# Kernel tuning notes

Measured on AMD Instinct MI355X. Metric: run time of the kernel, lower is better.

Reference implementation:

```python
import jax, jax.numpy as jnp
import numpy as np


def setup_inputs() -> dict:
    key = jax.random.key(0)
    ks = jax.random.split(key, 5)
    S, B, H, L = 512, 64, 1024, 2
    scale = 0.1
    return {
        "x": jax.random.normal(ks[0], (S, B, H), dtype=jnp.float32),
        "h0": jnp.zeros((L, B, H), dtype=jnp.float32),
        "c0": jnp.zeros((L, B, H), dtype=jnp.float32),
        "Wx": jax.random.uniform(ks[1], (L, 4 * H, H), minval=-scale, maxval=scale, dtype=jnp.float32),
        "Wh": jax.random.uniform(ks[2], (L, 4 * H, H), minval=-scale, maxval=scale, dtype=jnp.float32),
        "bx": jax.random.uniform(ks[3], (L, 4 * H), minval=-scale, maxval=scale, dtype=jnp.float32),
        "bh": jax.random.uniform(ks[4], (L, 4 * H), minval=-scale, maxval=scale, dtype=jnp.float32),
    }


def _cell(x_t, h_prev, c_prev, Wx_l, Wh_l, bx_l, bh_l, H):
    # gates: [B, 4H]; chunk order per source: f, i, o, c_ex
    gates = x_t @ Wx_l.T + bx_l + h_prev @ Wh_l.T + bh_l
    f, i, o, c_ex = jnp.split(gates, 4, axis=1)
    f = jax.nn.sigmoid(f)
    i = jax.nn.sigmoid(i)
    o = jax.nn.sigmoid(o)
    c_ex = jnp.tanh(c_ex)
    c = f * c_prev + i * c_ex
    h = o * jnp.tanh(c)
    return h, c


def reference(x, h0, c0, Wx, Wh, bx, bh):
    # x: [S, B, H]; h0/c0: [L, B, H]; Wx/Wh: [L, 4H, H]; bx/bh: [L, 4H]
    L = h0.shape[0]
    H = h0.shape[-1]

    def step(carry, x_t):
        h_all, c_all = carry  # each [L, B, H]
        out = x_t
        hs, cs = [], []
        for l in range(L):  # small fixed layer count
            h, c = _cell(out, h_all[l], c_all[l], Wx[l], Wh[l], bx[l], bh[l], H)
            out = h  # dropout is identity in eval mode
            hs.append(h)
            cs.append(c)
        return (jnp.stack(hs, 0), jnp.stack(cs, 0)), out

    (h_fin, c_fin), ys = jax.lax.scan(step, (h0, c0), x)
    return ys, (h_fin, c_fin)
```

## Files before the change

kernel.cpp:

```cpp
#include <hip/hip_runtime.h>

typedef __bf16 bf16_t;
typedef __bf16 bf16x8 __attribute__((ext_vector_type(8)));
typedef __bf16 bf16x4 __attribute__((ext_vector_type(4)));
typedef float  f32x4  __attribute__((ext_vector_type(4)));
typedef unsigned long long u64;

#define S_LEN 512
#define BATCH 64
#define HID 1024
#define BH (BATCH*HID)
#define G4 (4*HID)
#define NBLK 256
#define LBLK 128
#define NTHR 512
#define CSTRIDE 32
#define NCHK 8

__device__ __forceinline__ float sigmoid_f(float x) { return 1.f / (1.f + __expf(-x)); }
__device__ __forceinline__ float tanh_f(float x) {
    float e = __expf(-2.f * fabsf(x));
    float t = (1.f - e) / (1.f + e);
    return x >= 0.f ? t : -t;
}

__device__ __forceinline__ bf16x8 cvt8(const float* p) {
    float4 a = *reinterpret_cast<const float4*>(p);
    float4 b = *reinterpret_cast<const float4*>(p + 4);
    bf16x8 r;
    r[0] = (bf16_t)a.x; r[1] = (bf16_t)a.y; r[2] = (bf16_t)a.z; r[3] = (bf16_t)a.w;
    r[4] = (bf16_t)b.x; r[5] = (bf16_t)b.y; r[6] = (bf16_t)b.z; r[7] = (bf16_t)b.w;
    return r;
}

__device__ __forceinline__ void wait_chunk(const unsigned* cp, unsigned thr) {
    if (__hip_atomic_load(cp, __ATOMIC_RELAXED, __HIP_MEMORY_SCOPE_AGENT) < thr) {
        do { __builtin_amdgcn_s_sleep(2); }
        while (__hip_atomic_load(cp, __ATOMIC_RELAXED, __HIP_MEMORY_SCOPE_AGENT) < thr);
    }
    asm volatile("" ::: "memory");
}

__device__ __forceinline__ void gemm_phase_chunked(
    const bf16_t* __restrict__ abase, const unsigned* __restrict__ cbase, unsigned thr,
    int grbase, const unsigned char* __restrict__ lds_w,
    int kh, int quad, int r16, int ff, f32x4& acc0, f32x4& acc1)
{
    bf16x8 af[8];
    wait_chunk(&cbase[(4 * kh) * CSTRIDE], thr);
    if (!ff) __builtin_amdgcn_fence(__ATOMIC_ACQUIRE, "agent");
    #pragma unroll
    for (int j = 0; j < 4; ++j)
        af[j] = *reinterpret_cast<const bf16x8*>(abase + j * 32);
    #pragma unroll
    for (int c = 0; c < 4; ++c) {
        if (c < 3) {
            wait_chunk(&cbase[(4 * kh + c + 1) * CSTRIDE], thr);
            if (!ff) __builtin_amdgcn_fence(__ATOMIC_ACQUIRE, "agent");
            #pragma unroll
            for (int j = 0; j < 4; ++j)
                af[((c + 1) & 1) * 4 + j] =
                    *reinterpret_cast<const bf16x8*>(abase + (4 * (c + 1) + j) * 32);
        }
        #pragma unroll
        for (int j = 0; j < 4; ++j) {
            int ks = 4 * c + j;
            int gr = grbase + kh * 64 + ks * 4 + quad;
            bf16x8 b0 = *reinterpret_cast<const bf16x8*>(&lds_w[gr * 512 + r16 * 16]);
            bf16x8 b1 = *reinterpret_cast<const bf16x8*>(&lds_w[gr * 512 + (16 + r16) * 16]);
            acc0 = __builtin_amdgcn_mfma_f32_16x16x32_bf16(af[(c & 1) * 4 + j], b0, acc0, 0, 0, 0);
            acc1 = __builtin_amdgcn_mfma_f32_16x16x32_bf16(af[(c & 1) * 4 + j], b1, acc1, 0, 0, 0);
        }
    }
}

__global__ void prep_kernel(const float* __restrict__ h0,
                            bf16_t* __restrict__ h0buf, bf16_t* __restrict__ h1buf,
                            unsigned* __restrict__ cnt, int mask0, int mask1) {
    int gtid = blockIdx.x * blockDim.x + threadIdx.x;
    int gsz  = gridDim.x * blockDim.x;
    if (gtid < 2 * NCHK) cnt[gtid * CSTRIDE] = 0u;
    for (int i = gtid; i < BH; i += gsz) {
        h0buf[(size_t)mask0 * BH + i] = (bf16_t)h0[i];
        h1buf[(size_t)mask1 * BH + i] = (bf16_t)h0[BH + i];
    }
}

__global__ __launch_bounds__(NTHR, 2) void lstm_persistent(
    const float* __restrict__ x,
    const float* __restrict__ c0,
    const float* __restrict__ Wx,
    const float* __restrict__ Wh,
    const float* __restrict__ bx,
    const float* __restrict__ bh,
    float* __restrict__ out,
    bf16_t* __restrict__ h0buf,
    bf16_t* __restrict__ h1buf,
    unsigned* __restrict__ cnt,
    int ff, int mask0, int mask1)
{
    __shared__ __attribute__((aligned(16))) unsigned char lds_w[256 * 512];
    __shared__ __attribute__((aligned(16))) float lds_red[8 * 256];
    __shared__ __attribute__((aligned(16))) float lds_hf[BATCH * 8];

    const int tid  = threadIdx.x;
    const int bid  = blockIdx.x;
    const int l    = bid >> 7;
    const int ug8  = bid & 127;
    const int lane = tid & 63;
    const int wv   = tid >> 6;
    const int mt   = wv >> 1;
    const int kh   = wv & 1;
    const int quad = lane >> 4;
    const int r16  = lane & 15;

    float* ys   = out;
    float* hfin = out + (size_t)S_LEN * BH;
    float* cfin = hfin + 2 * BH;

    {
        const float* WxL = Wx + (size_t)l * G4 * HID;
        const float* WhL = Wh + (size_t)l * G4 * HID;
        for (int ch = tid; ch < 32 * 256; ch += NTHR) {
            int row = ch & 31;
            int gr  = ch >> 5;
            int ul = row >> 2, g = row & 3;
            size_t R = (size_t)g * HID + 8 * ug8 + ul;
            const float* src = (gr < 128) ? (WxL + R * HID + (size_t)gr * 8)
                                          : (WhL + R * HID + (size_t)(gr - 128) * 8);
            *reinterpret_cast<bf16x8*>(&lds_w[gr * 512 + row * 16]) = cvt8(src);
        }
    }

    const int b_loc  = lane >> 2;
    const int uu     = lane & 3;
    const int b_glob = 16 * mt + b_loc;
    const int u_loc  = 4 * kh + uu;
    const int u_glob = 8 * ug8 + u_loc;

    float bias_r[4];
    #pragma unroll
    for (int gi = 0; gi < 4; ++gi) {
        int R = gi * HID + u_glob;
        bias_r[gi] = bx[l * G4 + R] + bh[l * G4 + R];
    }
    float c_reg = c0[(size_t)l * BH + (size_t)b_glob * HID + u_glob];

    bf16_t* pubbuf = (l == 0) ? h0buf : h1buf;
    const int pubmask = (l == 0) ? mask0 : mask1;
    const unsigned* cnt0 = cnt;
    const unsigned* cnt1 = cnt + NCHK * CSTRIDE;
    unsigned* mycnt = &cnt[(l * NCHK + (ug8 >> 4)) * CSTRIDE];
    __syncthreads();

    const int arow_off = (16 * mt + r16) * HID + kh * 512 + quad * 8;

    bf16x8 axp[16];
    if (l == 0) {
        const float* arow = x + arow_off;
        #pragma unroll
        for (int ks = 0; ks < 16; ++ks) axp[ks] = cvt8(arow + ks * 32);
    }

    for (int t = 0; t < S_LEN; ++t) {
        f32x4 acc0 = {0.f, 0.f, 0.f, 0.f};
        f32x4 acc1 = {0.f, 0.f, 0.f, 0.f};

        if (l == 0) {
            #pragma unroll
            for (int ks = 0; ks < 16; ++ks) {
                int gr = kh * 64 + ks * 4 + quad;
                bf16x8 b0 = *reinterpret_cast<const bf16x8*>(&lds_w[gr * 512 + r16 * 16]);
                bf16x8 b1 = *reinterpret_cast<const bf16x8*>(&lds_w[gr * 512 + (16 + r16) * 16]);
                acc0 = __builtin_amdgcn_mfma_f32_16x16x32_bf16(axp[ks], b0, acc0, 0, 0, 0);
                acc1 = __builtin_amdgcn_mfma_f32_16x16x32_bf16(axp[ks], b1, acc1, 0, 0, 0);
            }
            const bf16_t* ah = h0buf + (size_t)((t - 1) & mask0) * BH + arow_off;
            gemm_phase_chunked(ah, cnt0, (unsigned)(16 * t), 128, lds_w,
                               kh, quad, r16, ff, acc0, acc1);
        } else {
            const bf16_t* ax = h0buf + (size_t)(t & mask0) * BH + arow_off;
            gemm_phase_chunked(ax, cnt0, (unsigned)(16 * (t + 1)), 0, lds_w,
                               kh, quad, r16, ff, acc0, acc1);
            const bf16_t* ah = h1buf + (size_t)((t - 1) & mask1) * BH + arow_off;
            gemm_phase_chunked(ah, cnt1, (unsigned)(16 * t), 128, lds_w,
                               kh, quad, r16, ff, acc0, acc1);
        }

        {
            f32x4 ship = kh ? acc0 : acc1;
            *reinterpret_cast<f32x4*>(&lds_red[wv * 256 + lane * 4]) = ship;
            __syncthreads();
            f32x4 part = *reinterpret_cast<const f32x4*>(&lds_red[(wv ^ 1) * 256 + lane * 4]);
            f32x4 keep = kh ? acc1 : acc0;
            acc0 = keep + part;
        }

        {
            const int quad_s = b_loc >> 2;
            const int reg_s  = b_loc & 3;
            float gsum[4];
            #pragma unroll
            for (int gi = 0; gi < 4; ++gi) {
                int lane_s = (quad_s << 4) | (4 * uu + gi);
                float v0 = __shfl(acc0[0], lane_s, 64);
                float v1 = __shfl(acc0[1], lane_s, 64);
                float v2 = __shfl(acc0[2], lane_s, 64);
                float v3 = __shfl(acc0[3], lane_s, 64);
                float v  = (reg_s == 0) ? v0 : (reg_s == 1) ? v1 : (reg_s == 2) ? v2 : v3;
                gsum[gi] = v + bias_r[gi];
            }
            float fg = sigmoid_f(gsum[0]);
            float ig = sigmoid_f(gsum[1]);
            float og = sigmoid_f(gsum[2]);
            float cx = tanh_f(gsum[3]);
            float cN = fg * c_reg + ig * cx;
            float h  = og * tanh_f(cN);
            c_reg = cN;
            lds_hf[b_glob * 8 + u_loc] = h;
            if (t == S_LEN - 1) {
                hfin[(size_t)l * BH + (size_t)b_glob * HID + u_glob] = h;
                cfin[(size_t)l * BH + (size_t)b_glob * HID + u_glob] = cN;
            }
        }
        __syncthreads();

        if (tid < 64) {
            if (!ff && l == 0 && t >= 8) {
                #pragma unroll
                for (int c = 0; c < NCHK; ++c)
                    wait_chunk(&cnt1[c * CSTRIDE], (unsigned)(16 * (t - 6)));
            }
            const float* hp = &lds_hf[lane * 8];
            union { bf16x4 v; u64 q; } p0, p1;
            #pragma unroll
            for (int j = 0; j < 4; ++j) {
                p0.v[j] = (bf16_t)hp[j];
                p1.v[j] = (bf16_t)hp[4 + j];
            }
            bf16_t* dst = pubbuf + (size_t)(t & pubmask) * BH + (size_t)lane * HID + 8 * ug8;
            __hip_atomic_store((u64*)(void*)dst,       p0.q, __ATOMIC_RELAXED, __HIP_MEMORY_SCOPE_AGENT);
            __hip_atomic_store((u64*)(void*)(dst + 4), p1.q, __ATOMIC_RELAXED, __HIP_MEMORY_SCOPE_AGENT);
            asm volatile("s_waitcnt vmcnt(0)" ::: "memory");
            if (lane == 0)
                __hip_atomic_fetch_add(mycnt, 1u, __ATOMIC_RELAXED, __HIP_MEMORY_SCOPE_AGENT);
            if (l == 1) {
                float* yd = ys + (size_t)t * BH + (size_t)lane * HID + 8 * ug8;
                __builtin_nontemporal_store(*reinterpret_cast<const f32x4*>(hp),     reinterpret_cast<f32x4*>(yd));
                __builtin_nontemporal_store(*reinterpret_cast<const f32x4*>(hp + 4), reinterpret_cast<f32x4*>(yd + 4));
            }
        }

        if (l == 0 && t + 1 < S_LEN) {
            const float* arow = x + (size_t)(t + 1) * BH + arow_off;
            #pragma unroll
            for (int ks = 0; ks < 16; ++ks) axp[ks] = cvt8(arow + ks * 32);
        }
    }
}

extern "C" void kernel_launch(void* const* d_in, const int* in_sizes, int n_in,
                              void* d_out, int out_size, void* d_ws, size_t ws_size,
                              hipStream_t stream) {
    (void)in_sizes; (void)n_in; (void)out_size;
    const float* x  = (const float*)d_in[0];
    const float* h0 = (const float*)d_in[1];
    const float* c0 = (const float*)d_in[2];
    const float* Wx = (const float*)d_in[3];
    const float* Wh = (const float*)d_in[4];
    const float* bx = (const float*)d_in[5];
    const float* bh = (const float*)d_in[6];

    unsigned char* ws = (unsigned char*)d_ws;
    unsigned* cnt = (unsigned*)ws;
    size_t off = 32768;
    size_t need_ff = off + (size_t)2 * S_LEN * BH * 2;
    int ff, mask0, mask1;
    bf16_t *h0buf, *h1buf;
    if (ws_size >= need_ff) {
        ff = 1; mask0 = S_LEN - 1; mask1 = S_LEN - 1;
        h0buf = (bf16_t*)(ws + off); off += (size_t)S_LEN * BH * 2;
        h1buf = (bf16_t*)(ws + off);
    } else {
        ff = 0; mask0 = 7; mask1 = 1;
        h0buf = (bf16_t*)(ws + off); off += (size_t)8 * BH * 2;
        h1buf = (bf16_t*)(ws + off);
    }

    prep_kernel<<<2048, 256, 0, stream>>>(h0, h0buf, h1buf, cnt, mask0, mask1);
    lstm_persistent<<<NBLK, NTHR, 0, stream>>>(x, c0, Wx, Wh, bx, bh, (float*)d_out,
                                               h0buf, h1buf, cnt, ff, mask0, mask1);
}
```

Baseline: 6.419 ms.

## Replace shared atomic chunk counters with per-block step flags polled in parallel

Each producer block now publishes its completed timestep by storing to its own flag word, where before it did an atomic fetch_add on a counter shared by 16 blocks. Consumers poll the 16 flag words of a chunk in parallel across lanes and combine them with a wave vote. This removes atomic contention on shared counters and lowers the polling sleep. Layer 1 now waits on its own recurrent h first and on layer 0's output second, so the dependency that is more likely ready is taken later. The cost is more poll loads per wait.

```diff
diff --git a/kernel.cpp b/kernel.cpp
--- a/kernel.cpp
+++ b/kernel.cpp
@@ -15,7 +15,6 @@
 #define LBLK 128
 #define NTHR 512
 #define CSTRIDE 32
-#define NCHK 8
 
 __device__ __forceinline__ float sigmoid_f(float x) { return 1.f / (1.f + __expf(-x)); }
 __device__ __forceinline__ float tanh_f(float x) {
@@ -33,21 +32,25 @@
     return r;
 }
 
-__device__ __forceinline__ void wait_chunk(const unsigned* cp, unsigned thr) {
-    if (__hip_atomic_load(cp, __ATOMIC_RELAXED, __HIP_MEMORY_SCOPE_AGENT) < thr) {
-        do { __builtin_amdgcn_s_sleep(2); }
-        while (__hip_atomic_load(cp, __ATOMIC_RELAXED, __HIP_MEMORY_SCOPE_AGENT) < thr);
+__device__ __forceinline__ void wait_words(const unsigned* dw, int cc, unsigned thr, int lane) {
+    const unsigned* p = dw + (size_t)(16 * cc + (lane & 15)) * CSTRIDE;
+    for (;;) {
+        unsigned v = thr;
+        if (lane < 16)
+            v = __hip_atomic_load(p, __ATOMIC_RELAXED, __HIP_MEMORY_SCOPE_AGENT);
+        if (__all((int)(v >= thr))) break;
+        __builtin_amdgcn_s_sleep(1);
     }
     asm volatile("" ::: "memory");
 }
 
 __device__ __forceinline__ void gemm_phase_chunked(
-    const bf16_t* __restrict__ abase, const unsigned* __restrict__ cbase, unsigned thr,
+    const bf16_t* __restrict__ abase, const unsigned* __restrict__ dwords, unsigned thr,
     int grbase, const unsigned char* __restrict__ lds_w,
-    int kh, int quad, int r16, int ff, f32x4& acc0, f32x4& acc1)
+    int kh, int quad, int r16, int lane, int ff, f32x4& acc0, f32x4& acc1)
 {
     bf16x8 af[8];
-    wait_chunk(&cbase[(4 * kh) * CSTRIDE], thr);
+    wait_words(dwords, 4 * kh, thr, lane);
     if (!ff) __builtin_amdgcn_fence(__ATOMIC_ACQUIRE, "agent");
     #pragma unroll
     for (int j = 0; j < 4; ++j)
@@ -55,7 +58,7 @@
     #pragma unroll
     for (int c = 0; c < 4; ++c) {
         if (c < 3) {
-            wait_chunk(&cbase[(4 * kh + c + 1) * CSTRIDE], thr);
+            wait_words(dwords, 4 * kh + c + 1, thr, lane);
             if (!ff) __builtin_amdgcn_fence(__ATOMIC_ACQUIRE, "agent");
             #pragma unroll
             for (int j = 0; j < 4; ++j)
@@ -76,10 +79,10 @@
 
 __global__ void prep_kernel(const float* __restrict__ h0,
                             bf16_t* __restrict__ h0buf, bf16_t* __restrict__ h1buf,
-                            unsigned* __restrict__ cnt, int mask0, int mask1) {
+                            unsigned* __restrict__ dw, int mask0, int mask1) {
     int gtid = blockIdx.x * blockDim.x + threadIdx.x;
     int gsz  = gridDim.x * blockDim.x;
-    if (gtid < 2 * NCHK) cnt[gtid * CSTRIDE] = 0u;
+    if (gtid < 2 * LBLK) dw[gtid * CSTRIDE] = 0u;
     for (int i = gtid; i < BH; i += gsz) {
         h0buf[(size_t)mask0 * BH + i] = (bf16_t)h0[i];
         h1buf[(size_t)mask1 * BH + i] = (bf16_t)h0[BH + i];
@@ -96,7 +99,7 @@
     float* __restrict__ out,
     bf16_t* __restrict__ h0buf,
     bf16_t* __restrict__ h1buf,
-    unsigned* __restrict__ cnt,
+    unsigned* __restrict__ dw,
     int ff, int mask0, int mask1)
 {
     __shared__ __attribute__((aligned(16))) unsigned char lds_w[256 * 512];
@@ -148,9 +151,9 @@
 
     bf16_t* pubbuf = (l == 0) ? h0buf : h1buf;
     const int pubmask = (l == 0) ? mask0 : mask1;
-    const unsigned* cnt0 = cnt;
-    const unsigned* cnt1 = cnt + NCHK * CSTRIDE;
-    unsigned* mycnt = &cnt[(l * NCHK + (ug8 >> 4)) * CSTRIDE];
+    const unsigned* dw0 = dw;
+    const unsigned* dw1 = dw + LBLK * CSTRIDE;
+    unsigned* myword = &dw[(l * LBLK + ug8) * CSTRIDE];
     __syncthreads();
 
     const int arow_off = (16 * mt + r16) * HID + kh * 512 + quad * 8;
@@ -176,15 +179,15 @@
                 acc1 = __builtin_amdgcn_mfma_f32_16x16x32_bf16(axp[ks], b1, acc1, 0, 0, 0);
             }
             const bf16_t* ah = h0buf + (size_t)((t - 1) & mask0) * BH + arow_off;
-            gemm_phase_chunked(ah, cnt0, (unsigned)(16 * t), 128, lds_w,
-                               kh, quad, r16, ff, acc0, acc1);
+            gemm_phase_chunked(ah, dw0, (unsigned)t, 128, lds_w,
+                               kh, quad, r16, lane, ff, acc0, acc1);
         } else {
+            const bf16_t* ah = h1buf + (size_t)((t - 1) & mask1) * BH + arow_off;
+            gemm_phase_chunked(ah, dw1, (unsigned)t, 128, lds_w,
+                               kh, quad, r16, lane, ff, acc0, acc1);
             const bf16_t* ax = h0buf + (size_t)(t & mask0) * BH + arow_off;
-            gemm_phase_chunked(ax, cnt0, (unsigned)(16 * (t + 1)), 0, lds_w,
-                               kh, quad, r16, ff, acc0, acc1);
-            const bf16_t* ah = h1buf + (size_t)((t - 1) & mask1) * BH + arow_off;
-            gemm_phase_chunked(ah, cnt1, (unsigned)(16 * t), 128, lds_w,
-                               kh, quad, r16, ff, acc0, acc1);
+            gemm_phase_chunked(ax, dw0, (unsigned)(t + 1), 0, lds_w,
+                               kh, quad, r16, lane, ff, acc0, acc1);
         }
 
         {
@@ -227,9 +230,15 @@
 
         if (tid < 64) {
             if (!ff && l == 0 && t >= 8) {
-                #pragma unroll
-                for (int c = 0; c < NCHK; ++c)
-                    wait_chunk(&cnt1[c * CSTRIDE], (unsigned)(16 * (t - 6)));
+                const unsigned thr = (unsigned)(t - 6);
+                for (;;) {
+                    unsigned v0 = __hip_atomic_load(&dw1[lane * CSTRIDE],
+                                                    __ATOMIC_RELAXED, __HIP_MEMORY_SCOPE_AGENT);
+                    unsigned v1 = __hip_atomic_load(&dw1[(64 + lane) * CSTRIDE],
+                                                    __ATOMIC_RELAXED, __HIP_MEMORY_SCOPE_AGENT);
+                    if (__all((int)(v0 >= thr && v1 >= thr))) break;
+                    __builtin_amdgcn_s_sleep(1);
+                }
             }
             const float* hp = &lds_hf[lane * 8];
             union { bf16x4 v; u64 q; } p0, p1;
@@ -243,7 +252,8 @@
             __hip_atomic_store((u64*)(void*)(dst + 4), p1.q, __ATOMIC_RELAXED, __HIP_MEMORY_SCOPE_AGENT);
             asm volatile("s_waitcnt vmcnt(0)" ::: "memory");
             if (lane == 0)
-                __hip_atomic_fetch_add(mycnt, 1u, __ATOMIC_RELAXED, __HIP_MEMORY_SCOPE_AGENT);
+                __hip_atomic_store(myword, (unsigned)(t + 1),
+                                   __ATOMIC_RELAXED, __HIP_MEMORY_SCOPE_AGENT);
             if (l == 1) {
                 float* yd = ys + (size_t)t * BH + (size_t)lane * HID + 8 * ug8;
                 __builtin_nontemporal_store(*reinterpret_cast<const f32x4*>(hp),     reinterpret_cast<f32x4*>(yd));
@@ -272,7 +282,7 @@
     const float* bh = (const float*)d_in[6];
 
     unsigned char* ws = (unsigned char*)d_ws;
-    unsigned* cnt = (unsigned*)ws;
+    unsigned* dw = (unsigned*)ws;
     size_t off = 32768;
     size_t need_ff = off + (size_t)2 * S_LEN * BH * 2;
     int ff, mask0, mask1;
@@ -287,7 +297,7 @@
         h1buf = (bf16_t*)(ws + off);
     }
 
-    prep_kernel<<<2048, 256, 0, stream>>>(h0, h0buf, h1buf, cnt, mask0, mask1);
+    prep_kernel<<<2048, 256, 0, stream>>>(h0, h0buf, h1buf, dw, mask0, mask1);
     lstm_persistent<<<NBLK, NTHR, 0, stream>>>(x, c0, Wx, Wh, bx, bh, (float*)d_out,
-                                               h0buf, h1buf, cnt, ff, mask0, mask1);
-}
+                                               h0buf, h1buf, dw, ff, mask0, mask1);
+}
```

Result: no change. 6.470 ms (+0.8%).
